# Kernel optimization log

Measured on AMD Instinct MI355X. Metric: run time of the kernel, lower is better.

The kernel has to match this reference:

```python
import jax, jax.numpy as jnp
import numpy as np

T1, T2 = 234, 234
N_HEAD = 16

def _cross_mask(t1, t2):
    # Faithful to the torch code: mask is FLOAT, so torch SDPA treats it as an
    # ADDITIVE bias (+1.0 on cross-image positions and on row/col 0, +0 elsewhere).
    T = t1 + t2
    m = np.zeros((T, T), dtype=np.float32)
    m[:t1, t1:] = 1.0
    m[t1:, :t1] = 1.0
    full = np.ones((T + 1, T + 1), dtype=np.float32)
    full[1:, 1:] = m
    return jnp.asarray(full)

CROSS_MASK = _cross_mask(T1, T2)  # (469, 469) additive bias

def setup_inputs() -> dict:
    key = jax.random.key(0)
    ks = jax.random.split(key, 5)
    B, T, C = 64, T1 + T2 + 1, 1024
    s = 0.02
    return {
        "x": jax.random.normal(ks[0], (B, T, C), jnp.float32),
        "W_attn": jax.random.normal(ks[1], (C, 3 * C), jnp.float32) * s,
        "b_attn": jax.random.normal(ks[2], (3 * C,), jnp.float32) * s,
        "W_proj": jax.random.normal(ks[3], (C, C), jnp.float32) * s,
        "b_proj": jax.random.normal(ks[4], (C,), jnp.float32) * s,
    }

def reference(x, W_attn, b_attn, W_proj, b_proj):
    B, T, C = x.shape
    H = N_HEAD
    hd = C // H
    qkv = x @ W_attn + b_attn                      # (B, T, 3C)
    q, k, v = jnp.split(qkv, 3, axis=-1)
    def heads(t):                                  # (B, T, C) -> (B, H, T, hd)
        return t.reshape(B, T, H, hd).transpose(0, 2, 1, 3)
    q, k, v = heads(q), heads(k), heads(v)
    scale = 1.0 / jnp.sqrt(jnp.asarray(hd, x.dtype))
    scores = jnp.einsum('bhqd,bhkd->bhqk', q, k) * scale + CROSS_MASK[None, None]
    attn = jax.nn.softmax(scores, axis=-1)
    y = jnp.einsum('bhqk,bhkd->bhqd', attn, v)     # (B, H, T, hd)
    y = y.transpose(0, 2, 1, 3).reshape(B, T, C)
    return y @ W_proj + b_proj
```

## Files before the change

### kernel.cpp

```cpp
#include <hip/hip_runtime.h>

namespace {

constexpr int kT1   = 234;
constexpr int kT    = 469;
constexpr int kB    = 64;
constexpr int kC    = 1024;
constexpr int kH    = 16;
constexpr int kHD   = 64;
constexpr int kM    = kB * kT;
constexpr int kVPad = 480;
constexpr float kC1 = 0.125f * 1.44269504089f;
constexpr float kC2 = 1.44269504089f;
constexpr float kShift = 4.0f * 1.44269504089f;
constexpr float kMC0 = -kShift;
constexpr float kMC1 = kC2 - kShift;
constexpr float kNeg = -30000.f;

typedef _Float16 f16;
typedef __fp16   fp16x2 __attribute__((ext_vector_type(2)));
typedef _Float16 f16x8 __attribute__((ext_vector_type(8)));
typedef float    f32x4 __attribute__((ext_vector_type(4)));

__device__ __forceinline__ float fast_exp2(float x) {
#if __has_builtin(__builtin_amdgcn_exp2f)
  return __builtin_amdgcn_exp2f(x);
#else
  return __builtin_exp2f(x);
#endif
}

__device__ __forceinline__ void gload16(const void* g, void* l) {
  __builtin_amdgcn_global_load_lds(
      (const __attribute__((address_space(1))) unsigned int*)g,
      (__attribute__((address_space(3))) unsigned int*)l, 16, 0, 0);
}

__global__ __launch_bounds__(256) void prep_kernel(
    const float* __restrict__ x, f16* __restrict__ xh,
    const float* __restrict__ Wa, f16* __restrict__ WaT,
    const float* __restrict__ Wp, f16* __restrict__ WpT, int n4) {
  __shared__ float tile[32][33];
  int b = blockIdx.x;
  if (b < 2048) {
    int i = b * blockDim.x + threadIdx.x;
    int stride = 2048 * blockDim.x;
    for (int j = i; j < n4; j += stride) {
      float4 v = reinterpret_cast<const float4*>(x)[j];
      union { f16 h[4]; unsigned long long u; } pk;
      pk.h[0] = (f16)v.x; pk.h[1] = (f16)v.y; pk.h[2] = (f16)v.z; pk.h[3] = (f16)v.w;
      reinterpret_cast<unsigned long long*>(xh)[j] = pk.u;
    }
    return;
  }
  const float* W; f16* Wt; int N0, i;
  if (b < 5120) { W = Wa; Wt = WaT; N0 = 3072; i = b - 2048; }
  else          { W = Wp; Wt = WpT; N0 = 1024; i = b - 5120; }
  int kb = (i & 31) * 32, nb = (i >> 5) * 32;
  int tx = threadIdx.x & 31, ty = threadIdx.x >> 5;
  #pragma unroll
  for (int r = ty; r < 32; r += 8) tile[r][tx] = W[(size_t)(kb + r) * N0 + nb + tx];
  __syncthreads();
  #pragma unroll
  for (int r = ty; r < 32; r += 8) Wt[(size_t)(nb + r) * 1024 + kb + tx] = (f16)tile[tx][r];
}

__global__ __launch_bounds__(256) void vtrans(const f16* __restrict__ in,
                                              f16* __restrict__ out) {
  __shared__ f16 tile[64][66];
  int bid = blockIdx.x;
  int bh = bid >> 3, tt = bid & 7;
  int t0 = tt * 64;
  int tx = threadIdx.x & 63, ty = threadIdx.x >> 6;
  const f16* src = in + (size_t)bh * kT * kHD;
  #pragma unroll
  for (int rr = ty; rr < 64; rr += 4) {
    int t = t0 + rr;
    tile[rr][tx] = (t < kT) ? src[(size_t)t * kHD + tx] : (f16)0.f;
  }
  __syncthreads();
  f16* dst = out + (size_t)bh * kHD * kVPad;
  int s = tx & 31, sub = tx >> 5;
  int tloc = sub * 32 + ((s >> 3) << 2) + (s & 3) + (((s >> 2) & 1) << 4);
  int tout = t0 + tx;
  if (tout < kVPad) {
    int pbase = tout & ~31, plo = tout & 7, pc = (tout >> 3) & 3;
    #pragma unroll
    for (int dd = ty; dd < 64; dd += 4) {
      int touts = pbase | plo | ((pc ^ ((dd >> 1) & 3)) << 3);
      dst[(size_t)dd * kVPad + touts] = tile[tloc][dd];
    }
  }
}

template <int EPI>
__global__ __launch_bounds__(512, 1) void gemm256(
    const f16* __restrict__ A, const f16* __restrict__ Bt,
    const float* __restrict__ bias,
    f16* __restrict__ qh, f16* __restrict__ kh, f16* __restrict__ vh,
    float* __restrict__ outp, int nbx, int nblocks) {
  __shared__ __align__(16) f16 SH[65536];
  const int K = 1024;
  int flat = blockIdx.x;
  int swz = (flat & 7) * (nblocks >> 3) + (flat >> 3);
  int mt = swz / nbx;
  int m0 = mt * 256, n0 = (swz - mt * nbx) * 256;
  int tid = threadIdx.x;
  int wid = tid >> 6, lane = tid & 63;
  int wm = wid >> 2, wn = wid & 3;
  int lhi = lane >> 4, llo = lane & 15;

  int ci0 = tid, ci1 = tid + 512;
  int r0 = ci0 >> 2, c0 = (ci0 & 3) ^ ((r0 >> 1) & 3);
  int r1 = ci1 >> 2, c1 = (ci1 & 3) ^ ((r1 >> 1) & 3);
  int gmA0 = m0 + r0; if (gmA0 >= kM) gmA0 = kM - 1;
  int gmA1 = m0 + r1; if (gmA1 >= kM) gmA1 = kM - 1;
  const f16* aS0 = A + (size_t)gmA0 * K + c0 * 8;
  const f16* aS1 = A + (size_t)gmA1 * K + c1 * 8;
  const f16* bS0 = Bt + (size_t)(n0 + r0) * K + c0 * 8;
  const f16* bS1 = Bt + (size_t)(n0 + r1) * K + c1 * 8;
  const int ld0 = ci0 * 8, ld1 = ci1 * 8;

  auto stage = [&](int reg, int kofs) {
    gload16(aS0 + kofs, &SH[reg + ld0]);
    gload16(aS1 + kofs, &SH[reg + ld1]);
    gload16(bS0 + kofs, &SH[32768 + reg + ld0]);
    gload16(bS1 + kofs, &SH[32768 + reg + ld1]);
  };

  int aOff[8], bOff[4];
  #pragma unroll
  for (int mi = 0; mi < 8; mi++) {
    int row = wm * 128 + mi * 16 + llo;
    aOff[mi] = row * 32 + ((lhi ^ ((row >> 1) & 3)) << 3);
  }
  #pragma unroll
  for (int ni = 0; ni < 4; ni++) {
    int row = wn * 64 + ni * 16 + llo;
    bOff[ni] = row * 32 + ((lhi ^ ((row >> 1) & 3)) << 3);
  }

  const f32x4 zero4 = {0.f, 0.f, 0.f, 0.f};
  f32x4 acc[8][4];
  #pragma unroll
  for (int mi = 0; mi < 8; mi++)
    #pragma unroll
    for (int ni = 0; ni < 4; ni++) acc[mi][ni] = zero4;

  stage(0 * 8192, 0);
  stage(1 * 8192, 32);
  stage(2 * 8192, 64);
  stage(3 * 8192, 96);

  for (int t = 0; t < 16; ++t) {
    int buf = t & 1;
    if (t < 15) asm volatile("s_waitcnt vmcnt(8)" ::: "memory");
    else        asm volatile("s_waitcnt vmcnt(4)" ::: "memory");
    __builtin_amdgcn_s_barrier();
    __builtin_amdgcn_sched_barrier(0);
    {
      int rb = (buf * 2 + 0) * 8192;
      f16x8 af[8], bf[4];
      #pragma unroll
      for (int mi = 0; mi < 8; mi++)
        af[mi] = *reinterpret_cast<const f16x8*>(&SH[rb + aOff[mi]]);
      #pragma unroll
      for (int ni = 0; ni < 4; ni++)
        bf[ni] = *reinterpret_cast<const f16x8*>(&SH[32768 + rb + bOff[ni]]);
      if (t >= 1 && t <= 14)
        stage(((buf ^ 1) * 2 + 1) * 8192, (t + 1) * 64 + 32);
      asm volatile("s_waitcnt lgkmcnt(0)" ::: "memory");
      __builtin_amdgcn_sched_barrier(0);
      __builtin_amdgcn_s_setprio(1);
      #pragma unroll
      for (int mi = 0; mi < 8; mi++)
        #pragma unroll
        for (int ni = 0; ni < 4; ni++)
          acc[mi][ni] = __builtin_amdgcn_mfma_f32_16x16x32_f16(af[mi], bf[ni], acc[mi][ni], 0, 0, 0);
      __builtin_amdgcn_s_setprio(0);
    }
    if (t < 15) asm volatile("s_waitcnt vmcnt(8)" ::: "memory");
    else        asm volatile("s_waitcnt vmcnt(0)" ::: "memory");
    __builtin_amdgcn_s_barrier();
    __builtin_amdgcn_sched_barrier(0);
    {
      int rb = (buf * 2 + 1) * 8192;
      f16x8 af[8], bf[4];
      #pragma unroll
      for (int mi = 0; mi < 8; mi++)
        af[mi] = *reinterpret_cast<const f16x8*>(&SH[rb + aOff[mi]]);
      #pragma unroll
      for (int ni = 0; ni < 4; ni++)
        bf[ni] = *reinterpret_cast<const f16x8*>(&SH[32768 + rb + bOff[ni]]);
      if (t <= 13)
        stage((buf * 2 + 0) * 8192, (t + 2) * 64);
      asm volatile("s_waitcnt lgkmcnt(0)" ::: "memory");
      __builtin_amdgcn_sched_barrier(0);
      __builtin_amdgcn_s_setprio(1);
      #pragma unroll
      for (int mi = 0; mi < 8; mi++)
        #pragma unroll
        for (int ni = 0; ni < 4; ni++)
          acc[mi][ni] = __builtin_amdgcn_mfma_f32_16x16x32_f16(af[mi], bf[ni], acc[mi][ni], 0, 0, 0);
      __builtin_amdgcn_s_setprio(0);
    }
  }

  float bsv[4];
  #pragma unroll
  for (int ni = 0; ni < 4; ni++) bsv[ni] = bias[n0 + wn * 64 + ni * 16 + llo];

  if constexpr (EPI == 0) {
    const int which = n0 >> 10;
    f16* dst = (which == 0) ? qh : (which == 1) ? kh : vh;
    const float osc = (which == 0) ? kC1 : 1.0f;
    #pragma unroll
    for (int mi = 0; mi < 8; mi++) {
      #pragma unroll
      for (int rr = 0; rr < 4; rr++) {
        int row = m0 + wm * 128 + mi * 16 + lhi * 4 + rr;
        if (row < kM) {
          int bb = row / kT;
          int t  = row - bb * kT;
          #pragma unroll
          for (int ni = 0; ni < 4; ni++) {
            int n = n0 + wn * 64 + ni * 16 + llo;
            int h = (n >> 6) & 15, d = n & 63;
            if (which == 1) d = (d & 7) | ((((d >> 3) ^ (t & 7)) & 7) << 3);
            dst[(((size_t)bb * kH + h) * kT + t) * kHD + d] =
                (f16)((acc[mi][ni][rr] + bsv[ni]) * osc);
          }
        }
      }
    }
  } else {
    #pragma unroll
    for (int mi = 0; mi < 8; mi++) {
      #pragma unroll
      for (int rr = 0; rr < 4; rr++) {
        int row = m0 + wm * 128 + mi * 16 + lhi * 4 + rr;
        if (row < kM) {
          #pragma unroll
          for (int ni = 0; ni < 4; ni++) {
            int n = n0 + wn * 64 + ni * 16 + llo;
            outp[(size_t)row * kC + n] = acc[mi][ni][rr] + bsv[ni];
          }
        }
      }
    }
  }
}

__global__ __launch_bounds__(512) void attn_kernel(
    const f16* __restrict__ qh, const f16* __restrict__ kh,
    const f16* __restrict__ vt, f16* __restrict__ y) {
  __shared__ __align__(16) f16 SH[24576];
  int tid = threadIdx.x;
  int w = tid >> 6, lane = tid & 63;
  int lhi = lane >> 4, llo = lane & 15;
  int bh = (blockIdx.x & 7) * 128 + (blockIdx.x >> 3);
  int bb = bh >> 4, h = bh & 15;
  const f16* qb = qh + (size_t)bh * kT * kHD;
  const f16* kb = kh + (size_t)bh * kT * kHD;
  const f16* vb = vt + (size_t)bh * kHD * kVPad;
  int qbase = w * 64;

  f16x8 qf[4][2];
  float mA[4], mB[4];
  #pragma unroll
  for (int rf = 0; rf < 4; rf++) {
    int qr = qbase + rf * 16 + llo;
    if (qr > kT - 1) qr = kT - 1;
    #pragma unroll
    for (int ks = 0; ks < 2; ks++)
      qf[rf][ks] = *reinterpret_cast<const f16x8*>(&qb[(size_t)qr * kHD + ks * 32 + lhi * 8]);
    int q = qbase + rf * 16 + llo;
    mA[rf] = (q == 0 || q > kT1) ? kMC1 : kMC0;
    mB[rf] = (q <= kT1) ? kMC1 : kMC0;
  }

  const bool isK = (tid < 256);
  const int vtid = tid & 255;
  const f16* kSrc = kb + (size_t)vtid * 8;
  const f16* vSrc = vb + (size_t)(vtid >> 2) * kVPad + (vtid & 3) * 8;
  const int ldsK = vtid * 8;
  const int ldsV = 2048 + vtid * 8;

  int kOff[2][2], vOff[4];
  #pragma unroll
  for (int kf = 0; kf < 2; kf++)
    #pragma unroll
    for (int ks = 0; ks < 2; ks++)
      kOff[kf][ks] = (kf * 16 + llo) * 64 + (((ks * 4 + lhi) ^ (llo & 7)) << 3);
  #pragma unroll
  for (int d = 0; d < 4; d++)
    vOff[d] = 2048 + (d * 16 + llo) * 32 + ((lhi ^ ((llo >> 1) & 3)) << 3);

  const f32x4 zero4 = {0.f, 0.f, 0.f, 0.f};
  f32x4 O[4][4];
  float lp[4] = {0.f, 0.f, 0.f, 0.f};
  #pragma unroll
  for (int rf = 0; rf < 4; rf++)
    #pragma unroll
    for (int d = 0; d < 4; d++) O[rf][d] = zero4;

  auto stage = [&](int t) {
    int reg = (t % 6) * 4096;
    if (isK) gload16(kSrc + (size_t)t * 2048, &SH[reg + ldsK]);
    else     gload16(vSrc + t * 32,           &SH[reg + ldsV]);
  };

  auto process = [&](int t) {
    int reg = (t % 6) * 4096;
    f16x8 kfr[2][2], vfr[4];
    #pragma unroll
    for (int kf = 0; kf < 2; kf++)
      #pragma unroll
      for (int ks = 0; ks < 2; ks++)
        kfr[kf][ks] = *reinterpret_cast<const f16x8*>(&SH[reg + kOff[kf][ks]]);
    __builtin_amdgcn_sched_barrier(0);
    #pragma unroll
    for (int d = 0; d < 4; d++)
      vfr[d] = *reinterpret_cast<const f16x8*>(&SH[reg + vOff[d]]);
    __builtin_amdgcn_sched_barrier(0);
    asm volatile("s_waitcnt lgkmcnt(4)" ::: "memory");
    __builtin_amdgcn_sched_barrier(0);

    f32x4 s[2][4];
    #pragma unroll
    for (int rf = 0; rf < 4; rf++) {
      float a = mA[rf], b = mB[rf];
      f32x4 sa = {a, a, a, a}, sb = {b, b, b, b};
      f32x4 s0, s1;
      if (t == 0) {
        s0 = sa; if (lhi == 0) s0[0] = kMC1;
        s1 = sa;
      } else if (t < 7) { s0 = sa; s1 = sa; }
      else if (t == 7) {
        f32x4 mix = {a, a, a, b};
        s0 = (lhi <= 1) ? sa : (lhi == 2) ? mix : sb;
        s1 = sb;
      } else if (t < 14) { s0 = sb; s1 = sb; }
      else {
        s0 = sb;
        f32x4 mix = {b, kNeg, kNeg, kNeg};
        f32x4 nng = {kNeg, kNeg, kNeg, kNeg};
        s1 = (lhi == 0) ? sb : (lhi == 1) ? mix : nng;
      }
      s[0][rf] = s0; s[1][rf] = s1;
    }

    __builtin_amdgcn_s_setprio(1);
    #pragma unroll
    for (int ks = 0; ks < 2; ks++)
      #pragma unroll
      for (int kf = 0; kf < 2; kf++)
        #pragma unroll
        for (int rf = 0; rf < 4; rf++)
          s[kf][rf] = __builtin_amdgcn_mfma_f32_16x16x32_f16(
              kfr[kf][ks], qf[rf][ks], s[kf][rf], 0, 0, 0);
    __builtin_amdgcn_s_setprio(0);

    f16x8 pa[4];
    #pragma unroll
    for (int rf = 0; rf < 4; rf++) {
      float p0 = fast_exp2(s[0][rf][0]), p1 = fast_exp2(s[0][rf][1]);
      float p2 = fast_exp2(s[0][rf][2]), p3 = fast_exp2(s[0][rf][3]);
      float p4 = fast_exp2(s[1][rf][0]), p5 = fast_exp2(s[1][rf][1]);
      float p6 = fast_exp2(s[1][rf][2]), p7 = fast_exp2(s[1][rf][3]);
      lp[rf] += ((p0 + p1) + (p2 + p3)) + ((p4 + p5) + (p6 + p7));
      union { fp16x2 h2[4]; f16x8 v; } u;
      u.h2[0] = __builtin_amdgcn_cvt_pkrtz(p0, p1);
      u.h2[1] = __builtin_amdgcn_cvt_pkrtz(p2, p3);
      u.h2[2] = __builtin_amdgcn_cvt_pkrtz(p4, p5);
      u.h2[3] = __builtin_amdgcn_cvt_pkrtz(p6, p7);
      pa[rf] = u.v;
    }

    asm volatile("s_waitcnt lgkmcnt(0)" ::: "memory");
    __builtin_amdgcn_sched_barrier(0);
    __builtin_amdgcn_s_setprio(1);
    #pragma unroll
    for (int d = 0; d < 4; d++)
      #pragma unroll
      for (int rf = 0; rf < 4; rf++)
        O[rf][d] = __builtin_amdgcn_mfma_f32_16x16x32_f16(pa[rf], vfr[d], O[rf][d], 0, 0, 0);
    __builtin_amdgcn_s_setprio(0);
  };

  stage(0); stage(1); stage(2); stage(3);

  for (int w2 = 0; w2 < 7; ++w2) {
    if (w2 < 6) asm volatile("s_waitcnt vmcnt(2)" ::: "memory");
    else        asm volatile("s_waitcnt vmcnt(1)" ::: "memory");
    __builtin_amdgcn_s_barrier();
    __builtin_amdgcn_sched_barrier(0);
    if (w2 <= 4)      { stage(2 * w2 + 4); stage(2 * w2 + 5); }
    else if (w2 == 5) { stage(14); }
    process(2 * w2);
    process(2 * w2 + 1);
  }
  asm volatile("s_waitcnt vmcnt(0)" ::: "memory");
  __builtin_amdgcn_s_barrier();
  __builtin_amdgcn_sched_barrier(0);
  process(14);

  #pragma unroll
  for (int rf = 0; rf < 4; rf++) {
    float l = lp[rf];
    l += __shfl_xor(l, 16, 64);
    l += __shfl_xor(l, 32, 64);
    #pragma unroll
    for (int r = 0; r < 4; r++) {
      float lr = __shfl(l, lhi * 4 + r, 64);
      int qi = qbase + rf * 16 + lhi * 4 + r;
      if (qi < kT) {
        float inv = 1.0f / lr;
        size_t base = ((size_t)bb * kT + qi) * kC + h * kHD;
        #pragma unroll
        for (int d = 0; d < 4; d++)
          y[base + d * 16 + llo] = (f16)(O[rf][d][r] * inv);
      }
    }
  }
}

}

extern "C" void kernel_launch(void* const* d_in, const int* in_sizes, int n_in,
                              void* d_out, int out_size, void* d_ws, size_t ws_size,
                              hipStream_t stream) {
  const float* x  = (const float*)d_in[0];
  const float* Wa = (const float*)d_in[1];
  const float* ba = (const float*)d_in[2];
  const float* Wp = (const float*)d_in[3];
  const float* bp = (const float*)d_in[4];
  float* out = (float*)d_out;
  char* ws = (char*)d_ws;

  const size_t sz_xh = (size_t)kM * kC * 2;
  const size_t sz_wa = (size_t)3072 * 1024 * 2;
  const size_t sz_wp = (size_t)1024 * 1024 * 2;
  const size_t sz_q  = (size_t)kB * kH * kT * kHD * 2;

  f16* xh  = (f16*)(ws);
  f16* WaT = (f16*)(ws + sz_xh);
  f16* WpT = (f16*)(ws + sz_xh + sz_wa);
  f16* qh  = (f16*)(ws + sz_xh + sz_wa + sz_wp);
  f16* kh2 = (f16*)(ws + sz_xh + sz_wa + sz_wp + sz_q);
  f16* vtt = (f16*)(ws + sz_xh + sz_wa + sz_wp + 2 * sz_q);
  f16* yh  = xh;
  f16* vtmp = (f16*)d_out;

  prep_kernel<<<6144, 256, 0, stream>>>(x, xh, Wa, WaT, Wp, WpT, kM * kC / 4);
  gemm256<0><<<118 * 12, 512, 0, stream>>>(xh, WaT, ba, qh, kh2, vtmp, nullptr, 12, 118 * 12);
  vtrans<<<kB * kH * 8, 256, 0, stream>>>(vtmp, vtt);
  attn_kernel<<<kB * kH, 512, 0, stream>>>(qh, kh2, vtt, yh);
  gemm256<1><<<118 * 4, 512, 0, stream>>>(yh, WpT, bp, nullptr, nullptr, nullptr, out, 4, 118 * 4);
}
```

Measured before the change: 529.2 us.

## Fuse V transpose into QKV GEMM epilogue and shrink attention LDS ring

The QKV GEMM epilogue now writes V directly into the transposed, swizzled padded layout that attention expects, which removes the separate vtrans kernel and its extra read and write of V. The attention kernel's K/V staging ring drops from six slots to four, with a one-tile-per-iteration loop and a prefetch depth of three. The fused V stores are strided by kVPad per d, so they coalesce worse in the GEMM epilogue. The smaller LDS footprint may allow higher occupancy, at the cost of less prefetch slack.

```diff
diff --git a/kernel.cpp b/kernel.cpp
--- a/kernel.cpp
+++ b/kernel.cpp
@@ -63,34 +63,6 @@
   __syncthreads();
   #pragma unroll
   for (int r = ty; r < 32; r += 8) Wt[(size_t)(nb + r) * 1024 + kb + tx] = (f16)tile[tx][r];
-}
-
-__global__ __launch_bounds__(256) void vtrans(const f16* __restrict__ in,
-                                              f16* __restrict__ out) {
-  __shared__ f16 tile[64][66];
-  int bid = blockIdx.x;
-  int bh = bid >> 3, tt = bid & 7;
-  int t0 = tt * 64;
-  int tx = threadIdx.x & 63, ty = threadIdx.x >> 6;
-  const f16* src = in + (size_t)bh * kT * kHD;
-  #pragma unroll
-  for (int rr = ty; rr < 64; rr += 4) {
-    int t = t0 + rr;
-    tile[rr][tx] = (t < kT) ? src[(size_t)t * kHD + tx] : (f16)0.f;
-  }
-  __syncthreads();
-  f16* dst = out + (size_t)bh * kHD * kVPad;
-  int s = tx & 31, sub = tx >> 5;
-  int tloc = sub * 32 + ((s >> 3) << 2) + (s & 3) + (((s >> 2) & 1) << 4);
-  int tout = t0 + tx;
-  if (tout < kVPad) {
-    int pbase = tout & ~31, plo = tout & 7, pc = (tout >> 3) & 3;
-    #pragma unroll
-    for (int dd = ty; dd < 64; dd += 4) {
-      int touts = pbase | plo | ((pc ^ ((dd >> 1) & 3)) << 3);
-      dst[(size_t)dd * kVPad + touts] = tile[tloc][dd];
-    }
-  }
 }
 
 template <int EPI>
@@ -212,23 +184,49 @@
 
   if constexpr (EPI == 0) {
     const int which = n0 >> 10;
-    f16* dst = (which == 0) ? qh : (which == 1) ? kh : vh;
-    const float osc = (which == 0) ? kC1 : 1.0f;
-    #pragma unroll
-    for (int mi = 0; mi < 8; mi++) {
-      #pragma unroll
-      for (int rr = 0; rr < 4; rr++) {
-        int row = m0 + wm * 128 + mi * 16 + lhi * 4 + rr;
-        if (row < kM) {
-          int bb = row / kT;
-          int t  = row - bb * kT;
-          #pragma unroll
-          for (int ni = 0; ni < 4; ni++) {
-            int n = n0 + wn * 64 + ni * 16 + llo;
-            int h = (n >> 6) & 15, d = n & 63;
-            if (which == 1) d = (d & 7) | ((((d >> 3) ^ (t & 7)) & 7) << 3);
-            dst[(((size_t)bb * kH + h) * kT + t) * kHD + d] =
-                (f16)((acc[mi][ni][rr] + bsv[ni]) * osc);
+    if (which == 2) {
+      const int hh = ((n0 >> 6) + wn) & 15;
+      #pragma unroll
+      for (int mi = 0; mi < 8; mi++) {
+        #pragma unroll
+        for (int rr = 0; rr < 4; rr++) {
+          int row = m0 + wm * 128 + mi * 16 + lhi * 4 + rr;
+          if (row < kM) {
+            int bb = row / kT;
+            int t  = row - bb * kT;
+            int lt = t & 31, tb = t & ~31;
+            int sstar = (((lt >> 4) & 1) << 2) | (((lt >> 3) & 1) << 4) |
+                        (((lt >> 2) & 1) << 3) | (lt & 3);
+            int plo = sstar & 7, pch = (sstar >> 3) & 3;
+            size_t vbase = (size_t)(bb * kH + hh) * kHD * kVPad;
+            #pragma unroll
+            for (int ni = 0; ni < 4; ni++) {
+              int d = ni * 16 + llo;
+              int touts = tb + plo + ((pch ^ ((d >> 1) & 3)) << 3);
+              vh[vbase + (size_t)d * kVPad + touts] = (f16)(acc[mi][ni][rr] + bsv[ni]);
+            }
+          }
+        }
+      }
+    } else {
+      f16* dst = (which == 0) ? qh : kh;
+      const float osc = (which == 0) ? kC1 : 1.0f;
+      #pragma unroll
+      for (int mi = 0; mi < 8; mi++) {
+        #pragma unroll
+        for (int rr = 0; rr < 4; rr++) {
+          int row = m0 + wm * 128 + mi * 16 + lhi * 4 + rr;
+          if (row < kM) {
+            int bb = row / kT;
+            int t  = row - bb * kT;
+            #pragma unroll
+            for (int ni = 0; ni < 4; ni++) {
+              int n = n0 + wn * 64 + ni * 16 + llo;
+              int h = (n >> 6) & 15, d = n & 63;
+              if (which == 1) d = (d & 7) | ((((d >> 3) ^ (t & 7)) & 7) << 3);
+              dst[(((size_t)bb * kH + h) * kT + t) * kHD + d] =
+                  (f16)((acc[mi][ni][rr] + bsv[ni]) * osc);
+            }
           }
         }
       }
@@ -254,7 +252,7 @@
 __global__ __launch_bounds__(512) void attn_kernel(
     const f16* __restrict__ qh, const f16* __restrict__ kh,
     const f16* __restrict__ vt, f16* __restrict__ y) {
-  __shared__ __align__(16) f16 SH[24576];
+  __shared__ __align__(16) f16 SH[16384];
   int tid = threadIdx.x;
   int w = tid >> 6, lane = tid & 63;
   int lhi = lane >> 4, llo = lane & 15;
@@ -305,13 +303,23 @@
     for (int d = 0; d < 4; d++) O[rf][d] = zero4;
 
   auto stage = [&](int t) {
-    int reg = (t % 6) * 4096;
+    int reg = (t & 3) * 4096;
     if (isK) gload16(kSrc + (size_t)t * 2048, &SH[reg + ldsK]);
     else     gload16(vSrc + t * 32,           &SH[reg + ldsV]);
   };
 
-  auto process = [&](int t) {
-    int reg = (t % 6) * 4096;
+  stage(0);
+  stage(1);
+  stage(2);
+
+  for (int t = 0; t < 15; ++t) {
+    if (t < 13)       asm volatile("s_waitcnt vmcnt(2)" ::: "memory");
+    else if (t == 13) asm volatile("s_waitcnt vmcnt(1)" ::: "memory");
+    else              asm volatile("s_waitcnt vmcnt(0)" ::: "memory");
+    __builtin_amdgcn_s_barrier();
+    __builtin_amdgcn_sched_barrier(0);
+    if (t <= 11) stage(t + 3);
+    int reg = (t & 3) * 4096;
     f16x8 kfr[2][2], vfr[4];
     #pragma unroll
     for (int kf = 0; kf < 2; kf++)
@@ -386,24 +394,7 @@
       for (int rf = 0; rf < 4; rf++)
         O[rf][d] = __builtin_amdgcn_mfma_f32_16x16x32_f16(pa[rf], vfr[d], O[rf][d], 0, 0, 0);
     __builtin_amdgcn_s_setprio(0);
-  };
-
-  stage(0); stage(1); stage(2); stage(3);
-
-  for (int w2 = 0; w2 < 7; ++w2) {
-    if (w2 < 6) asm volatile("s_waitcnt vmcnt(2)" ::: "memory");
-    else        asm volatile("s_waitcnt vmcnt(1)" ::: "memory");
-    __builtin_amdgcn_s_barrier();
-    __builtin_amdgcn_sched_barrier(0);
-    if (w2 <= 4)      { stage(2 * w2 + 4); stage(2 * w2 + 5); }
-    else if (w2 == 5) { stage(14); }
-    process(2 * w2);
-    process(2 * w2 + 1);
-  }
-  asm volatile("s_waitcnt vmcnt(0)" ::: "memory");
-  __builtin_amdgcn_s_barrier();
-  __builtin_amdgcn_sched_barrier(0);
-  process(14);
+  }
 
   #pragma unroll
   for (int rf = 0; rf < 4; rf++) {
@@ -450,11 +441,9 @@
   f16* kh2 = (f16*)(ws + sz_xh + sz_wa + sz_wp + sz_q);
   f16* vtt = (f16*)(ws + sz_xh + sz_wa + sz_wp + 2 * sz_q);
   f16* yh  = xh;
-  f16* vtmp = (f16*)d_out;
 
   prep_kernel<<<6144, 256, 0, stream>>>(x, xh, Wa, WaT, Wp, WpT, kM * kC / 4);
-  gemm256<0><<<118 * 12, 512, 0, stream>>>(xh, WaT, ba, qh, kh2, vtmp, nullptr, 12, 118 * 12);
-  vtrans<<<kB * kH * 8, 256, 0, stream>>>(vtmp, vtt);
+  gemm256<0><<<118 * 12, 512, 0, stream>>>(xh, WaT, ba, qh, kh2, vtt, nullptr, 12, 118 * 12);
   attn_kernel<<<kB * kH, 512, 0, stream>>>(qh, kh2, vtt, yh);
   gemm256<1><<<118 * 4, 512, 0, stream>>>(yh, WpT, bp, nullptr, nullptr, nullptr, out, 4, 118 * 4);
 }
```

Measured after the change: 500.4 us. -5.4%, faster.
